# Kernel optimization log

Measured on AMD Instinct MI355X. Metric: run time of the kernel, lower is better.

Reference implementation:

```python
import jax, jax.numpy as jnp
import numpy as np

C = 256
NH = 8
G = 32  # groupnorm groups (min(32, C))
EPS = 1e-6


def setup_inputs() -> dict:
    key = jax.random.key(0)
    ks = jax.random.split(key, 7)
    B, D, H, W = 2, 16, 16, 16
    x = jax.random.normal(ks[0], (B, C, D, H, W), dtype=jnp.float32)
    gn_gamma = jnp.ones((C,), jnp.float32)
    gn_beta = jnp.zeros((C,), jnp.float32)
    s = 1.0 / np.sqrt(C)
    qkv_w = jax.random.normal(ks[1], (3 * C, C), jnp.float32) * s  # 1x1x1 conv weight
    qkv_b = jnp.zeros((3 * C,), jnp.float32)
    proj_w = jax.random.normal(ks[2], (C, C), jnp.float32) * s
    proj_b = jnp.zeros((C,), jnp.float32)
    return {"x": x, "gn_gamma": gn_gamma, "gn_beta": gn_beta,
            "qkv_w": qkv_w, "qkv_b": qkv_b, "proj_w": proj_w, "proj_b": proj_b}


def _group_norm(x, gamma, beta):
    # x: [B, C, S]
    B, Cc, S = x.shape
    xg = x.reshape(B, G, (Cc // G) * S)
    mu = xg.mean(axis=-1, keepdims=True)
    var = xg.var(axis=-1, keepdims=True)
    xg = (xg - mu) * jax.lax.rsqrt(var + EPS)
    x = xg.reshape(B, Cc, S)
    return x * gamma[None, :, None] + beta[None, :, None]


def reference(x, gn_gamma, gn_beta, qkv_w, qkv_b, proj_w, proj_b):
    B, Cc, D, H, W = x.shape
    S = D * H * W
    hd = Cc // NH
    xf = x.reshape(B, Cc, S)
    h = _group_norm(xf, gn_gamma, gn_beta)
    # 1x1x1 conv == channel matmul: [B, 3C, S]
    qkv = jnp.einsum('oc,bcs->bos', qkv_w, h) + qkv_b[None, :, None]
    # torch path: reshape(B,3C,S).permute(0,2,1).chunk -> q=channels[0:C]
    q, k, v = qkv[:, :Cc], qkv[:, Cc:2 * Cc], qkv[:, 2 * Cc:]
    # [B, C, S] -> [B, NH, S, hd]
    def to_heads(t):
        return t.reshape(B, NH, hd, S).transpose(0, 1, 3, 2)
    q, k, v = to_heads(q), to_heads(k), to_heads(v)
    scale = hd ** (-0.5)
    attn = jax.nn.softmax(jnp.einsum('bnqd,bnkd->bnqk', q, k) * scale, axis=-1)
    o = jnp.einsum('bnqk,bnkd->bnqd', attn, v)  # [B, NH, S, hd]
    o = o.transpose(0, 1, 3, 2).reshape(B, Cc, S)  # back to [B, C, S]
    o = jnp.einsum('oc,bcs->bos', proj_w, o) + proj_b[None, :, None]
    return x + o.reshape(B, Cc, D, H, W)
```

## Files before the change

### kernel.cpp

```cpp
#include <hip/hip_runtime.h>
#include <cstddef>

#define S_LEN 4096
#define C_DIM 256
#define NHEADS 8
#define HDIM 32

typedef __attribute__((ext_vector_type(8))) _Float16 half8;
typedef __attribute__((ext_vector_type(4))) _Float16 half4;
typedef __attribute__((ext_vector_type(2))) _Float16 h2t;
typedef __attribute__((ext_vector_type(2))) __fp16 fp16x2;
typedef __attribute__((ext_vector_type(4))) float floatx4;

#define SC2F ((float)(0.17677669529663687 * 1.4426950408889634))

__global__ __launch_bounds__(256) void prep_stats(
    const float* __restrict__ qkv_w, const float* __restrict__ proj_w,
    const float* __restrict__ qkv_b, const float* __restrict__ x,
    _Float16* __restrict__ wq, _Float16* __restrict__ wp,
    float* __restrict__ qbias, float* __restrict__ pstat)
{
  const int blk = blockIdx.x;
  const int tid = threadIdx.x;
  if (blk < 512) {
    __shared__ float red[2][4];
    const int gb = blk >> 3, e = blk & 7;
    const int g = gb & 31, b = gb >> 5;
    const float* xb = x + ((size_t)b * C_DIM + g * 8) * S_LEN + e * 4096;
    const float4* x4 = (const float4*)xb;
    float sum = 0.f, sumsq = 0.f;
    #pragma unroll
    for (int i = 0; i < 4; ++i) {
      float4 v = x4[tid + i * 256];
      sum += v.x + v.y + v.z + v.w;
      sumsq += v.x * v.x + v.y * v.y + v.z * v.z + v.w * v.w;
    }
    for (int off = 1; off < 64; off <<= 1) {
      sum += __shfl_xor(sum, off, 64);
      sumsq += __shfl_xor(sumsq, off, 64);
    }
    const int wv = tid >> 6, lane = tid & 63;
    if (lane == 0) { red[0][wv] = sum; red[1][wv] = sumsq; }
    __syncthreads();
    if (tid == 0) {
      pstat[(gb * 8 + e) * 2 + 0] = red[0][0] + red[0][1] + red[0][2] + red[0][3];
      pstat[(gb * 8 + e) * 2 + 1] = red[1][0] + red[1][1] + red[1][2] + red[1][3];
    }
  } else {
    int idx = (blk - 512) * 256 + tid;
    if (idx < 768 * 256) {
      float v = qkv_w[idx];
      if (idx < 256 * 256) v *= SC2F;
      wq[idx] = (_Float16)v;
    } else if (idx < 768 * 256 + 256 * 256) {
      int i = idx - 768 * 256;
      wp[i] = (_Float16)proj_w[i];
    } else if (idx < 768 * 256 + 256 * 256 + 768) {
      int i = idx - (768 * 256 + 256 * 256);
      float bv = qkv_b[i];
      if (i < 256) bv *= SC2F;
      qbias[i] = bv;
    }
  }
}

__global__ __launch_bounds__(256) void qkv_gn_gemm(
    const _Float16* __restrict__ W, const float* __restrict__ bias,
    const float* __restrict__ x, const float* __restrict__ gamma,
    const float* __restrict__ beta, const float* __restrict__ pstat,
    _Float16* __restrict__ qo, _Float16* __restrict__ ko_,
    _Float16* __restrict__ vo)
{
  __shared__ __align__(16) _Float16 Ld[64 * 264];
  const int tid = threadIdx.x;
  const int b = blockIdx.z;
  const int s0 = blockIdx.y * 64;

  {
    const int c0 = (tid & 127) * 2, c1 = c0 + 1;
    const int sh = tid >> 7;
    const int g = c0 >> 3;
    const int gb = b * 32 + g;
    float s = 0.f, sq = 0.f;
    #pragma unroll
    for (int e = 0; e < 8; ++e) {
      s  += pstat[(gb * 8 + e) * 2 + 0];
      sq += pstat[(gb * 8 + e) * 2 + 1];
    }
    const float mean = s * (1.f / 32768.f);
    const float rstd = rsqrtf(sq * (1.f / 32768.f) - mean * mean + 1e-6f);
    const float ga0 = gamma[c0] * rstd, be0 = beta[c0] - mean * ga0;
    const float ga1 = gamma[c1] * rstd, be1 = beta[c1] - mean * ga1;
    const float4* xa = (const float4*)(x + ((size_t)b * C_DIM + c0) * S_LEN + s0 + sh * 32);
    const float4* xc = (const float4*)(x + ((size_t)b * C_DIM + c1) * S_LEN + s0 + sh * 32);
    #pragma unroll
    for (int j = 0; j < 8; ++j) {
      float4 a = xa[j], c = xc[j];
      int sl = sh * 32 + j * 4;
      *(h2t*)&Ld[(sl + 0) * 264 + c0] = (h2t){ (_Float16)(a.x * ga0 + be0), (_Float16)(c.x * ga1 + be1) };
      *(h2t*)&Ld[(sl + 1) * 264 + c0] = (h2t){ (_Float16)(a.y * ga0 + be0), (_Float16)(c.y * ga1 + be1) };
      *(h2t*)&Ld[(sl + 2) * 264 + c0] = (h2t){ (_Float16)(a.z * ga0 + be0), (_Float16)(c.z * ga1 + be1) };
      *(h2t*)&Ld[(sl + 3) * 264 + c0] = (h2t){ (_Float16)(a.w * ga0 + be0), (_Float16)(c.w * ga1 + be1) };
    }
  }
  __syncthreads();

  const int lane = tid & 63, wv = tid >> 6;
  const int m = lane & 15, quad = lane >> 4;
  const int mtb = blockIdx.x * 8 + wv * 2;
  const _Float16* wrow0 = W + (size_t)((mtb + 0) * 16 + m) * C_DIM + quad * 8;
  const _Float16* wrow1 = W + (size_t)((mtb + 1) * 16 + m) * C_DIM + quad * 8;
  const _Float16* lp = &Ld[m * 264 + quad * 8];

  floatx4 acc[2][4];
  #pragma unroll
  for (int j = 0; j < 2; ++j)
    #pragma unroll
    for (int s = 0; s < 4; ++s) acc[j][s] = (floatx4){0.f,0.f,0.f,0.f};

  #pragma unroll
  for (int k0 = 0; k0 < C_DIM; k0 += 32) {
    half8 b0 = *(const half8*)(lp + k0);
    half8 b1 = *(const half8*)(lp + 16 * 264 + k0);
    half8 b2 = *(const half8*)(lp + 32 * 264 + k0);
    half8 b3 = *(const half8*)(lp + 48 * 264 + k0);
    half8 a0 = *(const half8*)(wrow0 + k0);
    half8 a1 = *(const half8*)(wrow1 + k0);
    acc[0][0] = __builtin_amdgcn_mfma_f32_16x16x32_f16(a0, b0, acc[0][0], 0, 0, 0);
    acc[0][1] = __builtin_amdgcn_mfma_f32_16x16x32_f16(a0, b1, acc[0][1], 0, 0, 0);
    acc[0][2] = __builtin_amdgcn_mfma_f32_16x16x32_f16(a0, b2, acc[0][2], 0, 0, 0);
    acc[0][3] = __builtin_amdgcn_mfma_f32_16x16x32_f16(a0, b3, acc[0][3], 0, 0, 0);
    acc[1][0] = __builtin_amdgcn_mfma_f32_16x16x32_f16(a1, b0, acc[1][0], 0, 0, 0);
    acc[1][1] = __builtin_amdgcn_mfma_f32_16x16x32_f16(a1, b1, acc[1][1], 0, 0, 0);
    acc[1][2] = __builtin_amdgcn_mfma_f32_16x16x32_f16(a1, b2, acc[1][2], 0, 0, 0);
    acc[1][3] = __builtin_amdgcn_mfma_f32_16x16x32_f16(a1, b3, acc[1][3], 0, 0, 0);
  }

  if (blockIdx.x < 4) {
    #pragma unroll
    for (int j = 0; j < 2; ++j) {
      const int ob = (mtb + j) * 16 + quad * 4;
      const float bv0 = bias[ob], bv1 = bias[ob + 1],
                  bv2 = bias[ob + 2], bv3 = bias[ob + 3];
      #pragma unroll
      for (int sub = 0; sub < 4; ++sub) {
        int s = s0 + sub * 16 + m;
        half4 h = { (_Float16)(acc[j][sub][0] + bv0), (_Float16)(acc[j][sub][1] + bv1),
                    (_Float16)(acc[j][sub][2] + bv2), (_Float16)(acc[j][sub][3] + bv3) };
        _Float16* dst = (ob < 256) ? qo : ko_;
        int oo = ob & 255, n = oo >> 5, d0 = oo & 31;
        *(half4*)(dst + (((size_t)b * NHEADS + n) * S_LEN + s) * HDIM + d0) = h;
      }
    }
  } else {
    __syncthreads();
    _Float16* VLd = Ld;
    #pragma unroll
    for (int j = 0; j < 2; ++j) {
      const int ob = (mtb + j) * 16 + quad * 4;
      const int lch = (wv * 2 + j) * 16 + quad * 4;
      const float bv0 = bias[ob], bv1 = bias[ob + 1],
                  bv2 = bias[ob + 2], bv3 = bias[ob + 3];
      #pragma unroll
      for (int sub = 0; sub < 4; ++sub) {
        int s = sub * 16 + m;
        VLd[(lch + 0) * 72 + s] = (_Float16)(acc[j][sub][0] + bv0);
        VLd[(lch + 1) * 72 + s] = (_Float16)(acc[j][sub][1] + bv1);
        VLd[(lch + 2) * 72 + s] = (_Float16)(acc[j][sub][2] + bv2);
        VLd[(lch + 3) * 72 + s] = (_Float16)(acc[j][sub][3] + bv3);
      }
    }
    __syncthreads();
    const int lch = tid >> 1, sh = tid & 1;
    const int oo = (blockIdx.x - 4) * 128 + lch;
    const int n = oo >> 5, d = oo & 31;
    _Float16* dst = vo + ((size_t)(b * NHEADS + n) * HDIM + d) * S_LEN + s0 + sh * 32;
    const _Float16* src = VLd + lch * 72 + sh * 32;
    *(half8*)(dst + 0)  = *(const half8*)(src + 0);
    *(half8*)(dst + 8)  = *(const half8*)(src + 8);
    *(half8*)(dst + 16) = *(const half8*)(src + 16);
    *(half8*)(dst + 24) = *(const half8*)(src + 24);
  }
}

__global__ __launch_bounds__(512) void attn_kernel(
    const _Float16* __restrict__ q, const _Float16* __restrict__ k,
    const _Float16* __restrict__ v, _Float16* __restrict__ po,
    float* __restrict__ pl)
{
  __shared__ __align__(16) _Float16 Kl[2][64 * 40];
  __shared__ __align__(16) _Float16 Vl[2][32 * 68];
  const int tid = threadIdx.x;
  const int lane = tid & 63, wv = tid >> 6;
  const int m = lane & 15, quad = lane >> 4;
  const int n = blockIdx.y, b = blockIdx.z;
  const int qc = blockIdx.x >> 1, kh = blockIdx.x & 1;
  const int q0 = qc * 256 + wv * 32;
  const int bh = b * NHEADS + n;

  const _Float16* qb = q + (size_t)bh * S_LEN * HDIM;
  const _Float16* kb = k + (size_t)bh * S_LEN * HDIM + (size_t)kh * 2048 * HDIM;
  const _Float16* vb = v + (size_t)bh * HDIM * S_LEN + (size_t)kh * 2048;

  half8 qfA = *(const half8*)(qb + (size_t)(q0 + m) * HDIM + quad * 8);
  half8 qfB = *(const half8*)(qb + (size_t)(q0 + 16 + m) * HDIM + quad * 8);

  const int krow = wv * 8 + (lane >> 3), kc = (lane & 7) * 4;
  const int vrow = wv * 4 + (lane >> 4), vc = (lane & 15) * 4;
  const _Float16* kg = kb + (size_t)krow * HDIM + kc;
  const _Float16* vg = vb + (size_t)vrow * S_LEN + vc;
  const int klds = krow * 40 + kc;
  const int vlds = vrow * 68 + vc;

  int2 kreg = *(const int2*)kg;
  int2 vreg = *(const int2*)vg;
  const _Float16* kgp = kg + 64 * HDIM;
  const _Float16* vgp = vg + 64;

  floatx4 oA0 = {0.f,0.f,0.f,0.f}, oA1 = oA0, oB0 = oA0, oB1 = oA0;
  float lA = 0.f, lB = 0.f;
  const fp16x2 one2 = { (__fp16)1.0f, (__fp16)1.0f };

  #pragma unroll 2
  for (int it = 0; it < 32; ++it) {
    const int bufi = it & 1;
    *(int2*)(&Kl[bufi][klds]) = kreg;
    *(int2*)(&Vl[bufi][vlds]) = vreg;
    kreg = *(const int2*)kgp; kgp += 64 * HDIM;
    vreg = *(const int2*)vgp; vgp += 64;
    __syncthreads();
    const _Float16* Kb = Kl[bufi];
    const _Float16* Vb = Vl[bufi];
    #pragma unroll
    for (int t = 0; t < 4; ++t) {
      half8 kf = *(const half8*)(Kb + (t * 16 + m) * 40 + quad * 8);
      half4 vf0 = *(const half4*)(Vb + m * 68 + t * 16 + quad * 4);
      half4 vf1 = *(const half4*)(Vb + (16 + m) * 68 + t * 16 + quad * 4);
      floatx4 z = {0.f,0.f,0.f,0.f};
      floatx4 sA = __builtin_amdgcn_mfma_f32_16x16x32_f16(kf, qfA, z, 0, 0, 0);
      floatx4 sB = __builtin_amdgcn_mfma_f32_16x16x32_f16(kf, qfB, z, 0, 0, 0);
      float eA0 = __builtin_amdgcn_exp2f(sA[0]);
      float eA1 = __builtin_amdgcn_exp2f(sA[1]);
      float eA2 = __builtin_amdgcn_exp2f(sA[2]);
      float eA3 = __builtin_amdgcn_exp2f(sA[3]);
      float eB0 = __builtin_amdgcn_exp2f(sB[0]);
      float eB1 = __builtin_amdgcn_exp2f(sB[1]);
      float eB2 = __builtin_amdgcn_exp2f(sB[2]);
      float eB3 = __builtin_amdgcn_exp2f(sB[3]);
      half4 pA, pB;
      fp16x2 pAlo = __builtin_amdgcn_cvt_pkrtz(eA0, eA1);
      fp16x2 pAhi = __builtin_amdgcn_cvt_pkrtz(eA2, eA3);
      fp16x2 pBlo = __builtin_amdgcn_cvt_pkrtz(eB0, eB1);
      fp16x2 pBhi = __builtin_amdgcn_cvt_pkrtz(eB2, eB3);
      *(fp16x2*)&pA = pAlo; *((fp16x2*)&pA + 1) = pAhi;
      *(fp16x2*)&pB = pBlo; *((fp16x2*)&pB + 1) = pBhi;
      lA = __builtin_amdgcn_fdot2(pAlo, one2, lA, false);
      lA = __builtin_amdgcn_fdot2(pAhi, one2, lA, false);
      lB = __builtin_amdgcn_fdot2(pBlo, one2, lB, false);
      lB = __builtin_amdgcn_fdot2(pBhi, one2, lB, false);
      oA0 = __builtin_amdgcn_mfma_f32_16x16x16f16(vf0, pA, oA0, 0, 0, 0);
      oA1 = __builtin_amdgcn_mfma_f32_16x16x16f16(vf1, pA, oA1, 0, 0, 0);
      oB0 = __builtin_amdgcn_mfma_f32_16x16x16f16(vf0, pB, oB0, 0, 0, 0);
      oB1 = __builtin_amdgcn_mfma_f32_16x16x16f16(vf1, pB, oB1, 0, 0, 0);
    }
  }
  lA += __shfl_xor(lA, 16, 64); lA += __shfl_xor(lA, 32, 64);
  lB += __shfl_xor(lB, 16, 64); lB += __shfl_xor(lB, 32, 64);
  _Float16* pobase = po + (size_t)kh * 2097152 + ((size_t)bh * S_LEN) * HDIM;
  {
    _Float16* poh = pobase + (size_t)(q0 + m) * HDIM;
    half4 h0 = { (_Float16)oA0[0], (_Float16)oA0[1], (_Float16)oA0[2], (_Float16)oA0[3] };
    half4 h1 = { (_Float16)oA1[0], (_Float16)oA1[1], (_Float16)oA1[2], (_Float16)oA1[3] };
    *(half4*)(poh + quad * 4) = h0;
    *(half4*)(poh + 16 + quad * 4) = h1;
    if (quad == 0) pl[(size_t)kh * 65536 + (size_t)bh * S_LEN + q0 + m] = lA;
  }
  {
    _Float16* poh = pobase + (size_t)(q0 + 16 + m) * HDIM;
    half4 h0 = { (_Float16)oB0[0], (_Float16)oB0[1], (_Float16)oB0[2], (_Float16)oB0[3] };
    half4 h1 = { (_Float16)oB1[0], (_Float16)oB1[1], (_Float16)oB1[2], (_Float16)oB1[3] };
    *(half4*)(poh + quad * 4) = h0;
    *(half4*)(poh + 16 + quad * 4) = h1;
    if (quad == 0) pl[(size_t)kh * 65536 + (size_t)bh * S_LEN + q0 + 16 + m] = lB;
  }
}

__global__ __launch_bounds__(256) void proj_gemm(
    const _Float16* __restrict__ W, const float* __restrict__ bias,
    const _Float16* __restrict__ po, const float* __restrict__ pl,
    const float* __restrict__ x, float* __restrict__ out)
{
  __shared__ float Linv[512];
  const int tid = threadIdx.x;
  const int lane = tid & 63, wv = tid >> 6;
  const int m = lane & 15, quad = lane >> 4;
  const int mt = blockIdx.x * 4 + wv;
  const int s0 = blockIdx.y * 64;
  const int b = blockIdx.z;
  const int row = mt * 16 + m;

  {
    const int nn = tid >> 5, jj = (tid & 31) * 2;
    size_t base = (size_t)(b * NHEADS + nn) * S_LEN + s0 + jj;
    float a0 = pl[base]     + pl[65536 + base];
    float a1 = pl[base + 1] + pl[65536 + base + 1];
    Linv[nn * 64 + jj]     = 1.f / a0;
    Linv[nn * 64 + jj + 1] = 1.f / a1;
  }
  __syncthreads();

  const _Float16* wrow = W + (size_t)row * C_DIM + quad * 8;
  floatx4 acc0 = {0.f,0.f,0.f,0.f}, acc1 = acc0, acc2 = acc0, acc3 = acc0;
  #pragma unroll
  for (int k0 = 0; k0 < C_DIM; k0 += 32) {
    const int n = k0 >> 5;
    const int d0 = quad * 8;
    half8 bf[4];
    #pragma unroll
    for (int sub = 0; sub < 4; ++sub) {
      size_t idx = (((size_t)(b * NHEADS + n)) * S_LEN + s0 + sub * 16 + m) * HDIM + d0;
      half8 a = *(const half8*)(po + idx);
      half8 c = *(const half8*)(po + 2097152 + idx);
      _Float16 iv = (_Float16)Linv[n * 64 + sub * 16 + m];
      bf[sub] = (a + c) * iv;
    }
    half8 af = *(const half8*)(wrow + k0);
    acc0 = __builtin_amdgcn_mfma_f32_16x16x32_f16(af, bf[0], acc0, 0, 0, 0);
    acc1 = __builtin_amdgcn_mfma_f32_16x16x32_f16(af, bf[1], acc1, 0, 0, 0);
    acc2 = __builtin_amdgcn_mfma_f32_16x16x32_f16(af, bf[2], acc2, 0, 0, 0);
    acc3 = __builtin_amdgcn_mfma_f32_16x16x32_f16(af, bf[3], acc3, 0, 0, 0);
  }
  floatx4 accs[4] = {acc0, acc1, acc2, acc3};
  #pragma unroll
  for (int sub = 0; sub < 4; ++sub) {
    int s = s0 + sub * 16 + m;
    #pragma unroll
    for (int r = 0; r < 4; ++r) {
      int c = mt * 16 + quad * 4 + r;
      size_t idx = ((size_t)b * C_DIM + c) * S_LEN + s;
      out[idx] = x[idx] + accs[sub][r] + bias[c];
    }
  }
}

extern "C" void kernel_launch(void* const* d_in, const int* in_sizes, int n_in,
                              void* d_out, int out_size, void* d_ws, size_t ws_size,
                              hipStream_t stream) {
  const float* x        = (const float*)d_in[0];
  const float* gn_gamma = (const float*)d_in[1];
  const float* gn_beta  = (const float*)d_in[2];
  const float* qkv_w    = (const float*)d_in[3];
  const float* qkv_b    = (const float*)d_in[4];
  const float* proj_w   = (const float*)d_in[5];
  const float* proj_b   = (const float*)d_in[6];
  float* out = (float*)d_out;

  const size_t n1 = (size_t)2 * S_LEN * C_DIM;
  char* ws = (char*)d_ws;
  _Float16* qx  = (_Float16*)ws;
  _Float16* kx  = qx + n1;
  _Float16* vx  = kx + n1;
  _Float16* wq  = vx + n1;
  _Float16* wp  = wq + 768 * 256;
  float*    qbias = (float*)(wp + 256 * 256);
  float*    pstat = qbias + 768;
  _Float16* po  = (_Float16*)(pstat + 1024);
  float*    pl  = (float*)(po + 2 * n1);

  prep_stats<<<1539, 256, 0, stream>>>(qkv_w, proj_w, qkv_b, x, wq, wp, qbias, pstat);
  qkv_gn_gemm<<<dim3(6, 64, 2), 256, 0, stream>>>(wq, qbias, x, gn_gamma, gn_beta, pstat, qx, kx, vx);
  attn_kernel<<<dim3(32, 8, 2), 512, 0, stream>>>(qx, kx, vx, po, pl);
  proj_gemm<<<dim3(4, 64, 2), 256, 0, stream>>>(wp, proj_b, po, pl, x, out);
}
```

Measured before the change: 151.0 us.

## Double K/V tile size in attention, stagger wave tiles, add MFMA priority hints

The attention kernel now stages 128 keys per iteration instead of 64, using 16-byte global loads and half as many barriers. Each wave starts its inner loop at a different sub-tile offset, which should spread LDS bank traffic across waves. The MFMA calls are wrapped in s_setprio so they can be scheduled ahead of other waves' work. The row-sum accumulators are split into independent chains to shorten the dependency chain. LDS use doubles, which may reduce occupancy.

```diff
diff --git a/kernel.cpp b/kernel.cpp
--- a/kernel.cpp
+++ b/kernel.cpp
@@ -188,8 +188,8 @@
     const _Float16* __restrict__ v, _Float16* __restrict__ po,
     float* __restrict__ pl)
 {
-  __shared__ __align__(16) _Float16 Kl[2][64 * 40];
-  __shared__ __align__(16) _Float16 Vl[2][32 * 68];
+  __shared__ __align__(16) _Float16 Kl[2][128 * 40];
+  __shared__ __align__(16) _Float16 Vl[2][32 * 136];
   const int tid = threadIdx.x;
   const int lane = tid & 63, wv = tid >> 6;
   const int m = lane & 15, quad = lane >> 4;
@@ -205,40 +205,44 @@
   half8 qfA = *(const half8*)(qb + (size_t)(q0 + m) * HDIM + quad * 8);
   half8 qfB = *(const half8*)(qb + (size_t)(q0 + 16 + m) * HDIM + quad * 8);
 
-  const int krow = wv * 8 + (lane >> 3), kc = (lane & 7) * 4;
-  const int vrow = wv * 4 + (lane >> 4), vc = (lane & 15) * 4;
+  const int krow = wv * 16 + (lane >> 2), kc = (lane & 3) * 8;
+  const int vrow = wv * 4 + (lane >> 4), vc = (lane & 15) * 8;
   const _Float16* kg = kb + (size_t)krow * HDIM + kc;
   const _Float16* vg = vb + (size_t)vrow * S_LEN + vc;
   const int klds = krow * 40 + kc;
-  const int vlds = vrow * 68 + vc;
-
-  int2 kreg = *(const int2*)kg;
-  int2 vreg = *(const int2*)vg;
-  const _Float16* kgp = kg + 64 * HDIM;
-  const _Float16* vgp = vg + 64;
+  const int vlds = vrow * 136 + vc;
+
+  int4 kreg = *(const int4*)kg;
+  int4 vreg = *(const int4*)vg;
+  const _Float16* kgp = kg + 128 * HDIM;
+  const _Float16* vgp = vg + 128;
 
   floatx4 oA0 = {0.f,0.f,0.f,0.f}, oA1 = oA0, oB0 = oA0, oB1 = oA0;
-  float lA = 0.f, lB = 0.f;
+  float lA0 = 0.f, lA1 = 0.f, lB0 = 0.f, lB1 = 0.f;
   const fp16x2 one2 = { (__fp16)1.0f, (__fp16)1.0f };
+  const floatx4 zz = {0.f,0.f,0.f,0.f};
 
   #pragma unroll 2
-  for (int it = 0; it < 32; ++it) {
+  for (int it = 0; it < 16; ++it) {
     const int bufi = it & 1;
-    *(int2*)(&Kl[bufi][klds]) = kreg;
-    *(int2*)(&Vl[bufi][vlds]) = vreg;
-    kreg = *(const int2*)kgp; kgp += 64 * HDIM;
-    vreg = *(const int2*)vgp; vgp += 64;
+    *(int4*)(&Kl[bufi][klds]) = kreg;
+    *(int4*)(&Vl[bufi][vlds]) = vreg;
+    kreg = *(const int4*)kgp; kgp += 128 * HDIM;
+    vreg = *(const int4*)vgp; vgp += 128;
     __syncthreads();
     const _Float16* Kb = Kl[bufi];
     const _Float16* Vb = Vl[bufi];
-    #pragma unroll
-    for (int t = 0; t < 4; ++t) {
-      half8 kf = *(const half8*)(Kb + (t * 16 + m) * 40 + quad * 8);
-      half4 vf0 = *(const half4*)(Vb + m * 68 + t * 16 + quad * 4);
-      half4 vf1 = *(const half4*)(Vb + (16 + m) * 68 + t * 16 + quad * 4);
-      floatx4 z = {0.f,0.f,0.f,0.f};
-      floatx4 sA = __builtin_amdgcn_mfma_f32_16x16x32_f16(kf, qfA, z, 0, 0, 0);
-      floatx4 sB = __builtin_amdgcn_mfma_f32_16x16x32_f16(kf, qfB, z, 0, 0, 0);
+
+    #pragma unroll
+    for (int t = 0; t < 8; ++t) {
+      const int tt = (t + wv) & 7;
+      half8 kf  = *(const half8*)(Kb + (tt * 16 + m) * 40 + quad * 8);
+      half4 vf0 = *(const half4*)(Vb + m * 136 + tt * 16 + quad * 4);
+      half4 vf1 = *(const half4*)(Vb + (16 + m) * 136 + tt * 16 + quad * 4);
+      __builtin_amdgcn_s_setprio(1);
+      floatx4 sA = __builtin_amdgcn_mfma_f32_16x16x32_f16(kf, qfA, zz, 0, 0, 0);
+      floatx4 sB = __builtin_amdgcn_mfma_f32_16x16x32_f16(kf, qfB, zz, 0, 0, 0);
+      __builtin_amdgcn_s_setprio(0);
       float eA0 = __builtin_amdgcn_exp2f(sA[0]);
       float eA1 = __builtin_amdgcn_exp2f(sA[1]);
       float eA2 = __builtin_amdgcn_exp2f(sA[2]);
@@ -254,16 +258,19 @@
       fp16x2 pBhi = __builtin_amdgcn_cvt_pkrtz(eB2, eB3);
       *(fp16x2*)&pA = pAlo; *((fp16x2*)&pA + 1) = pAhi;
       *(fp16x2*)&pB = pBlo; *((fp16x2*)&pB + 1) = pBhi;
-      lA = __builtin_amdgcn_fdot2(pAlo, one2, lA, false);
-      lA = __builtin_amdgcn_fdot2(pAhi, one2, lA, false);
-      lB = __builtin_amdgcn_fdot2(pBlo, one2, lB, false);
-      lB = __builtin_amdgcn_fdot2(pBhi, one2, lB, false);
+      lA0 = __builtin_amdgcn_fdot2(pAlo, one2, lA0, false);
+      lA1 = __builtin_amdgcn_fdot2(pAhi, one2, lA1, false);
+      lB0 = __builtin_amdgcn_fdot2(pBlo, one2, lB0, false);
+      lB1 = __builtin_amdgcn_fdot2(pBhi, one2, lB1, false);
+      __builtin_amdgcn_s_setprio(1);
       oA0 = __builtin_amdgcn_mfma_f32_16x16x16f16(vf0, pA, oA0, 0, 0, 0);
       oA1 = __builtin_amdgcn_mfma_f32_16x16x16f16(vf1, pA, oA1, 0, 0, 0);
       oB0 = __builtin_amdgcn_mfma_f32_16x16x16f16(vf0, pB, oB0, 0, 0, 0);
       oB1 = __builtin_amdgcn_mfma_f32_16x16x16f16(vf1, pB, oB1, 0, 0, 0);
-    }
-  }
+      __builtin_amdgcn_s_setprio(0);
+    }
+  }
+  float lA = lA0 + lA1, lB = lB0 + lB1;
   lA += __shfl_xor(lA, 16, 64); lA += __shfl_xor(lA, 32, 64);
   lB += __shfl_xor(lB, 16, 64); lB += __shfl_xor(lB, 32, 64);
   _Float16* pobase = po + (size_t)kh * 2097152 + ((size_t)bh * S_LEN) * HDIM;
```

Result: no change. 148.3 us (-1.8%).
